# Performance work log

Hardware: AMD Instinct MI355X
Metric: run time of the kernel (lower is better)

The kernel has to match this reference:

```python
import jax, jax.numpy as jnp
import numpy as np
from math import sqrt

P = 1.0  # axis-aligned transform exponent (init arg p)
EPS = 1e-6


def setup_inputs() -> dict:
    key = jax.random.key(0)
    k1, k2, k3, k4 = jax.random.split(key, 4)
    B, L, S, H, E = 4, 2048, 2048, 8, 64
    return {
        "queries": jax.random.normal(k1, (B, L, H, E), dtype=jnp.float32),
        "keys": jax.random.normal(k2, (B, S, H, E), dtype=jnp.float32),
        "values": jax.random.normal(k3, (B, S, H, E), dtype=jnp.float32),
        "attn_mask": jnp.zeros((1, 1, 1, 1), dtype=bool),  # unused: mask_flag=False
        "directional_weights": jnp.ones((1, 1, 1, 1), dtype=jnp.float32),
        "dynamic_param": jax.random.normal(k4, (1,), dtype=jnp.float32),
    }


def _transform(x, directional_weights, dynamic_param):
    # axis_aligned_transformation: rescale by (1/std over seq dim)^p (unbiased std, like torch)
    std = jnp.std(x, axis=-2, keepdims=True, ddof=1)
    x = x * (1.0 / (std + EPS)) ** P
    # directional_reweighting then nonlinear_mapping
    x = x * directional_weights
    return jnp.tanh(x) * dynamic_param


def reference(queries, keys, values, attn_mask, directional_weights, dynamic_param):
    B, L, H, E = queries.shape
    scale = 1.0 / sqrt(E)
    qt = _transform(queries, directional_weights, dynamic_param)  # [B,L,H,E]
    kt = _transform(keys, directional_weights, dynamic_param)     # [B,S,H,E]
    scores = jnp.einsum('blhe,bshe->bhls', qt, kt)                # [B,H,L,S]
    # per-row tau = sqrt(var(scores) + eps), unbiased variance like torch.var
    tau = jnp.sqrt(jnp.var(scores, axis=-1, keepdims=True, ddof=1) + EPS)
    A = jax.nn.softmax(scale * scores / tau, axis=-1)             # [B,H,L,S]
    V = jnp.einsum('bhls,bshd->blhd', A, values)                  # [B,L,H,D]
    return V
```

## Files before the change

kernel.cpp:

```cpp
#include <hip/hip_runtime.h>
#include <math.h>

#define B_ 4
#define L_ 2048
#define S_ 2048
#define H_ 8
#define E_ 64
#define BH_ (B_*H_)
#define EPS 1e-6f
#define LOG2E 1.44269504088896340736f

typedef __attribute__((ext_vector_type(8))) short short8;
typedef __attribute__((ext_vector_type(4))) float f32x4;

__device__ __forceinline__ unsigned short f2bf(float f) {
    unsigned int u = __float_as_uint(f);
    u = (u + 0x7fffu + ((u >> 16) & 1u)) >> 16;
    return (unsigned short)u;
}

__device__ __forceinline__ float bf2f(unsigned short u) {
    return __uint_as_float(((unsigned int)u) << 16);
}

__device__ __forceinline__ float fast_tanh(float x) {
    float e = __expf(2.0f * x);
    return 1.0f - 2.0f / (e + 1.0f);
}

__device__ __forceinline__ unsigned int cvt_pk_bf16(float lo, float hi) {
    unsigned int r;
    asm("v_cvt_pk_bf16_f32 %0, %1, %2" : "=v"(r) : "v"(lo), "v"(hi));
    return r;
}
__device__ __forceinline__ float exp2_fast(float x) {
    float r;
    asm("v_exp_f32 %0, %1" : "=v"(r) : "v"(x));
    return r;
}
__device__ __forceinline__ void swap32(unsigned int &a, unsigned int &b) {
    asm("v_permlane32_swap_b32 %0, %1" : "+v"(a), "+v"(b));
}
__device__ __forceinline__ void swap16(unsigned int &a, unsigned int &b) {
    asm("v_permlane16_swap_b32 %0, %1" : "+v"(a), "+v"(b));
}

__device__ __forceinline__ int swb(int row, int byteoff) {
    return row * 128 + ((((byteoff >> 4) ^ (row & 7)) << 4) | (byteoff & 15));
}

__global__ __launch_bounds__(256) void pre_kernel(
    const float* __restrict__ xq, const float* __restrict__ xk,
    const float* __restrict__ xv,
    unsigned short* __restrict__ qt, unsigned short* __restrict__ kt,
    unsigned short* __restrict__ vt,
    const float* __restrict__ dwp, const float* __restrict__ dpp)
{
    __shared__ float ls[64][65];
    int bx = blockIdx.x;
    if (bx < 4096) {
        const float* x = (bx < 2048) ? xq : xk;
        unsigned short* xt = (bx < 2048) ? qt : kt;
        int g = (bx & 2047) * 256 + threadIdx.x;
        int e = g & 63;
        int bl = g >> 6;
        int b = bl >> 11;
        int l = bl & 2047;
        size_t base = (size_t)bl * (H_ * E_) + e;
        float v[8], s = 0.f, q = 0.f;
#pragma unroll
        for (int h = 0; h < 8; ++h) {
            float t = x[base + h * E_];
            v[h] = t; s += t; q += t * t;
        }
        float mean = s * 0.125f;
        float var = (q - s * mean) * (1.f / 7.f);
        var = fmaxf(var, 0.f);
        float inv = 1.f / (sqrtf(var) + EPS);
        float wsc = dwp[0] * inv;
        float d = dpp[0];
#pragma unroll
        for (int h = 0; h < 8; ++h) {
            float t = fast_tanh(v[h] * wsc) * d;
            xt[((size_t)(b * H_ + h) * L_ + l) * E_ + e] = f2bf(t);
        }
    } else {
        int t2 = bx - 4096;
        int s0 = (t2 & 31) * 64;
        int h = (t2 >> 5) & 7, b = t2 >> 8;
        int t = threadIdx.x;
#pragma unroll
        for (int i = 0; i < 4; ++i) {
            int idx = t + i * 256;
            int r = idx >> 4, c4 = (idx & 15) * 4;
            const float4 f = *(const float4*)&xv[((size_t)(b * S_ + s0 + r) * H_ + h) * E_ + c4];
            ls[r][c4] = f.x; ls[r][c4 + 1] = f.y; ls[r][c4 + 2] = f.z; ls[r][c4 + 3] = f.w;
        }
        __syncthreads();
        size_t ob = ((size_t)(b * H_ + h) * (S_ / 64) + (s0 >> 6)) * 4096;
#pragma unroll
        for (int i = 0; i < 2; ++i) {
            int ri = t + i * 256;
            int et = ri >> 7, c = (ri >> 6) & 1, quad = (ri >> 4) & 3, m = ri & 15;
            int e = et * 16 + m, sb = c * 32 + quad * 8;
            unsigned short tmp[8];
#pragma unroll
            for (int j = 0; j < 8; ++j) tmp[j] = f2bf(ls[sb + j][e]);
            *(uint4*)&vt[ob + (size_t)ri * 8] = *(uint4*)tmp;
        }
    }
}

__global__ __launch_bounds__(256) void gram_kernel(
    const unsigned short* __restrict__ kt, unsigned short* __restrict__ Gb,
    float* __restrict__ ksum)
{
    __shared__ unsigned short ks[128 * 72];
    __shared__ float gs[4096];
    __shared__ float kss[64];
    int bh = blockIdx.x;
    const unsigned short* base = kt + (size_t)bh * S_ * E_;
    int tid = threadIdx.x, lane = tid & 63, w = tid >> 6;
    int m = lane & 15, quad = lane >> 4;

    f32x4 acc[4][4];
#pragma unroll
    for (int i = 0; i < 4; ++i)
#pragma unroll
        for (int j = 0; j < 4; ++j) acc[i][j] = (f32x4){0.f, 0.f, 0.f, 0.f};
    float ksp[4] = {0.f, 0.f, 0.f, 0.f};

    short8 stg[4];
#pragma unroll
    for (int i = 0; i < 4; ++i)
        stg[i] = *(const short8*)(base + (size_t)(tid + i * 256) * 8);

    for (int ch = 0; ch < 16; ++ch) {
        __syncthreads();
#pragma unroll
        for (int i = 0; i < 4; ++i) {
            int u = tid + i * 256;
            *(short8*)&ks[(u >> 3) * 72 + (u & 7) * 8] = stg[i];
        }
        __syncthreads();
        if (ch < 15) {
#pragma unroll
            for (int i = 0; i < 4; ++i)
                stg[i] = *(const short8*)(base + (size_t)(ch + 1) * 8192 + (tid + i * 256) * 8);
        }
        int s0 = w * 32;
        short8 af[4];
#pragma unroll
        for (int i = 0; i < 4; ++i) {
            short8 a;
#pragma unroll
            for (int kk = 0; kk < 8; ++kk) {
                unsigned short uv = ks[(s0 + quad * 8 + kk) * 72 + i * 16 + m];
                a[kk] = (short)uv;
                ksp[i] += bf2f(uv);
            }
            af[i] = a;
        }
#pragma unroll
        for (int i = 0; i < 4; ++i)
#pragma unroll
            for (int j = 0; j < 4; ++j)
                acc[i][j] = __builtin_amdgcn_mfma_f32_16x16x32_bf16(af[i], af[j], acc[i][j], 0, 0, 0);
    }
#pragma unroll
    for (int i = 0; i < 4; ++i) {
        ksp[i] += __shfl_xor(ksp[i], 16);
        ksp[i] += __shfl_xor(ksp[i], 32);
    }
    for (int w2 = 0; w2 < 4; ++w2) {
        if (w == w2) {
#pragma unroll
            for (int i = 0; i < 4; ++i)
#pragma unroll
                for (int j = 0; j < 4; ++j)
#pragma unroll
                    for (int r = 0; r < 4; ++r) {
                        int idx = (i * 16 + quad * 4 + r) * 64 + j * 16 + m;
                        if (w2 == 0) gs[idx] = acc[i][j][r]; else gs[idx] += acc[i][j][r];
                    }
            if (lane < 16) {
#pragma unroll
                for (int i = 0; i < 4; ++i) {
                    int e = i * 16 + lane;
                    if (w2 == 0) kss[e] = ksp[i]; else kss[e] += ksp[i];
                }
            }
        }
        __syncthreads();
    }
#pragma unroll
    for (int ii = 0; ii < 16; ++ii) {
        int idx = tid + ii * 256;
        Gb[(size_t)bh * 4096 + idx] = f2bf(gs[idx]);
    }
    if (tid < 64) ksum[bh * 64 + tid] = kss[tid];
}

__global__ __launch_bounds__(512, 4) void attn_kernel(
    const unsigned short* __restrict__ qt,
    const unsigned short* __restrict__ kt,
    const unsigned short* __restrict__ vt,
    const unsigned short* __restrict__ Gb,
    const float* __restrict__ ksum,
    float* __restrict__ out)
{
    __shared__ __align__(16) char lds[17408];
    const int tid = threadIdx.x;
    const int lane = tid & 63;
    const int w = tid >> 6;
    const int m = lane & 15;
    const int quad = lane >> 4;
    float2* ascr = (float2*)(lds + 16384) + w * 16;

    int blk = blockIdx.x;
    int bh = (blk & 7) * 4 + ((blk >> 3) & 3);
    int l0 = (blk >> 5) * 128;
    int b = bh >> 3, h = bh & 7;

    const unsigned short* qtb = qt + (size_t)bh * L_ * E_;
    const unsigned short* ktb = kt + (size_t)bh * S_ * E_;
    const unsigned short* vtb = vt + (size_t)bh * (S_ / 64) * 4096;

    short8 qf[2];
#pragma unroll
    for (int c = 0; c < 2; ++c)
        qf[c] = *(const short8*)(qtb + (size_t)(l0 + w * 16 + m) * E_ + c * 32 + quad * 8);

    float al2, nalm2;
    {
        const unsigned short* gb = Gb + (size_t)bh * 4096;
        short8 gfr[4][2];
#pragma unroll
        for (int j = 0; j < 4; ++j)
#pragma unroll
            for (int c = 0; c < 2; ++c)
                gfr[j][c] = *(const short8*)(gb + (size_t)(j * 16 + m) * 64 + c * 32 + quad * 8);
        float ksl[4];
#pragma unroll
        for (int j = 0; j < 4; ++j) ksl[j] = ksum[bh * 64 + j * 16 + m];
        f32x4 accj[4];
#pragma unroll
        for (int j = 0; j < 4; ++j) {
            accj[j] = (f32x4){0.f, 0.f, 0.f, 0.f};
            accj[j] = __builtin_amdgcn_mfma_f32_16x16x32_bf16(qf[0], gfr[j][0], accj[j], 0, 0, 0);
            accj[j] = __builtin_amdgcn_mfma_f32_16x16x32_bf16(qf[1], gfr[j][1], accj[j], 0, 0, 0);
        }
        float ps[4] = {0, 0, 0, 0}, pr[4] = {0, 0, 0, 0};
#pragma unroll
        for (int r = 0; r < 4; ++r)
#pragma unroll
            for (int j = 0; j < 4; ++j) {
                float qv = bf2f(qtb[(size_t)(l0 + w * 16 + quad * 4 + r) * E_ + j * 16 + m]);
                ps[r] = fmaf(accj[j][r], qv, ps[r]);
                pr[r] = fmaf(qv, ksl[j], pr[r]);
            }
#pragma unroll
        for (int mask = 1; mask < 16; mask <<= 1)
#pragma unroll
            for (int r = 0; r < 4; ++r) {
                ps[r] += __shfl_xor(ps[r], mask);
                pr[r] += __shfl_xor(pr[r], mask);
            }
        if (m == 0) {
#pragma unroll
            for (int r = 0; r < 4; ++r) {
                float sum = pr[r];
                float mu = sum * (1.f / S_);
                float var = (ps[r] - sum * mu) * (1.f / (S_ - 1));
                var = fmaxf(var, 0.f);
                float tau = sqrtf(var + EPS);
                float a = 0.125f / tau;
                ascr[quad * 4 + r] = make_float2(a, a * mu);
            }
        }
        float2 a2 = ascr[m];
        al2 = a2.x * LOG2E; nalm2 = -a2.y * LOG2E;
    }

    f32x4 oacc[4];
#pragma unroll
    for (int et = 0; et < 4; ++et) oacc[et] = (f32x4){0.f, 0.f, 0.f, 0.f};
    f32x4 asum = (f32x4){0.f, 0.f, 0.f, 0.f};

    short8 ones;
#pragma unroll
    for (int j = 0; j < 8; ++j) ones[j] = (short)0x3F80;

    int ko[4];
#pragma unroll
    for (int nt = 0; nt < 4; ++nt)
        ko[nt] = swb(nt * 16 + m, quad * 16);
    const int stg = swb(tid >> 3, (tid & 7) * 16);

    uint4 kr = *(const uint4*)(ktb + (size_t)tid * 8);
    *(uint4*)(lds + stg) = kr;
    __syncthreads();

    auto step = [&](int st, char* kcur, char* knxt) {
        if (st < S_ / 64 - 1)
            kr = *(const uint4*)(ktb + (size_t)(st + 1) * 4096 + (size_t)tid * 8);
        const unsigned short* vstb = vtb + (size_t)st * 4096;
        short8 vf[2][4];
#pragma unroll
        for (int c = 0; c < 2; ++c)
#pragma unroll
            for (int et = 0; et < 4; ++et)
                vf[c][et] = *(const short8*)(vstb + et * 1024 + c * 512 + lane * 8);

        unsigned int W[4][2];
#pragma unroll
        for (int nt = 0; nt < 4; ++nt) {
            short8 kf0 = *(const short8*)(kcur + ko[nt]);
            short8 kf1 = *(const short8*)(kcur + (ko[nt] ^ 64));
            f32x4 acc = (f32x4){0.f, 0.f, 0.f, 0.f};
            acc = __builtin_amdgcn_mfma_f32_16x16x32_bf16(kf0, qf[0], acc, 0, 0, 0);
            acc = __builtin_amdgcn_mfma_f32_16x16x32_bf16(kf1, qf[1], acc, 0, 0, 0);
            float p0 = exp2_fast(fmaf(al2, acc[0], nalm2));
            float p1 = exp2_fast(fmaf(al2, acc[1], nalm2));
            float p2 = exp2_fast(fmaf(al2, acc[2], nalm2));
            float p3 = exp2_fast(fmaf(al2, acc[3], nalm2));
            W[nt][0] = cvt_pk_bf16(p0, p1);
            W[nt][1] = cvt_pk_bf16(p2, p3);
        }
        short8 pf[2];
#pragma unroll
        for (int c = 0; c < 2; ++c) {
            unsigned int a0 = W[2 * c][0], b0 = W[2 * c + 1][0];
            unsigned int a1 = W[2 * c][1], b1 = W[2 * c + 1][1];
            swap32(a0, b0); swap16(a0, b0);
            swap32(a1, b1); swap16(a1, b1);
            uint4 pk4;
            pk4.x = a0; pk4.y = a1; pk4.z = b0; pk4.w = b1;
            pf[c] = *(short8*)&pk4;
        }
#pragma unroll
        for (int et = 0; et < 4; ++et) {
            oacc[et] = __builtin_amdgcn_mfma_f32_16x16x32_bf16(pf[0], vf[0][et], oacc[et], 0, 0, 0);
            oacc[et] = __builtin_amdgcn_mfma_f32_16x16x32_bf16(pf[1], vf[1][et], oacc[et], 0, 0, 0);
        }
        asum = __builtin_amdgcn_mfma_f32_16x16x32_bf16(pf[0], ones, asum, 0, 0, 0);
        asum = __builtin_amdgcn_mfma_f32_16x16x32_bf16(pf[1], ones, asum, 0, 0, 0);
        if (st < S_ / 64 - 1)
            *(uint4*)(knxt + stg) = kr;
        __syncthreads();
    };
#pragma unroll 1
    for (int st2 = 0; st2 < S_ / 128; ++st2) {
        step(2 * st2,     lds,        lds + 8192);
        step(2 * st2 + 1, lds + 8192, lds);
    }

#pragma unroll
    for (int r = 0; r < 4; ++r) {
        float rd = 1.0f / asum[r];
        size_t row = (size_t)(b * L_ + l0 + w * 16 + quad * 4 + r);
#pragma unroll
        for (int et = 0; et < 4; ++et)
            out[(row * H_ + h) * E_ + et * 16 + m] = oacc[et][r] * rd;
    }
}

extern "C" void kernel_launch(void* const* d_in, const int* in_sizes, int n_in,
                              void* d_out, int out_size, void* d_ws, size_t ws_size,
                              hipStream_t stream)
{
    const float* q = (const float*)d_in[0];
    const float* k = (const float*)d_in[1];
    const float* v = (const float*)d_in[2];
    const float* dw = (const float*)d_in[4];
    const float* dp = (const float*)d_in[5];
    float* out = (float*)d_out;

    unsigned short* qt = (unsigned short*)d_ws;
    unsigned short* kt = qt + (size_t)BH_ * L_ * E_;
    unsigned short* vt = kt + (size_t)BH_ * S_ * E_;
    unsigned short* Gb = vt + (size_t)BH_ * E_ * S_;
    float* ksum = (float*)(Gb + (size_t)BH_ * 4096);

    pre_kernel<<<5120, 256, 0, stream>>>(q, k, v, qt, kt, vt, dw, dp);
    gram_kernel<<<BH_, 256, 0, stream>>>(kt, Gb, ksum);
    attn_kernel<<<512, 512, 0, stream>>>(qt, kt, vt, Gb, ksum, out);
}
```

Measured before the change: 168.8 us.

## Pre-swizzle K into MFMA fragment order and drop LDS staging in attention

The gram kernel now also writes K back in place in MFMA-fragment order. This lets the attention kernel load K fragments directly from global memory instead of staging them through double-buffered LDS with a barrier per step. Each wave now processes 32 query rows (two 16-row groups), so each K/V fragment load is reused twice, and blocks shrink to 256 threads. The pre kernel is also rewritten to use float4 loads and wave shuffles for the per-head std reduction, with packed bf16 stores. The risks are more redundant K traffic from L2 per wave, higher register pressure from the doubled accumulators, and an in-place layout rewrite that must stay ordered correctly within the gram kernel.

```diff
diff --git a/kernel.cpp b/kernel.cpp
--- a/kernel.cpp
+++ b/kernel.cpp
@@ -43,10 +43,6 @@
 }
 __device__ __forceinline__ void swap16(unsigned int &a, unsigned int &b) {
     asm("v_permlane16_swap_b32 %0, %1" : "+v"(a), "+v"(b));
-}
-
-__device__ __forceinline__ int swb(int row, int byteoff) {
-    return row * 128 + ((((byteoff >> 4) ^ (row & 7)) << 4) | (byteoff & 15));
 }
 
 __global__ __launch_bounds__(256) void pre_kernel(
@@ -58,37 +54,50 @@
 {
     __shared__ float ls[64][65];
     int bx = blockIdx.x;
+    int tid = threadIdx.x;
     if (bx < 4096) {
         const float* x = (bx < 2048) ? xq : xk;
         unsigned short* xt = (bx < 2048) ? qt : kt;
-        int g = (bx & 2047) * 256 + threadIdx.x;
-        int e = g & 63;
-        int bl = g >> 6;
-        int b = bl >> 11;
-        int l = bl & 2047;
-        size_t base = (size_t)bl * (H_ * E_) + e;
-        float v[8], s = 0.f, q = 0.f;
-#pragma unroll
-        for (int h = 0; h < 8; ++h) {
-            float t = x[base + h * E_];
-            v[h] = t; s += t; q += t * t;
-        }
-        float mean = s * 0.125f;
-        float var = (q - s * mean) * (1.f / 7.f);
-        var = fmaxf(var, 0.f);
-        float inv = 1.f / (sqrtf(var) + EPS);
-        float wsc = dwp[0] * inv;
-        float d = dpp[0];
-#pragma unroll
-        for (int h = 0; h < 8; ++h) {
-            float t = fast_tanh(v[h] * wsc) * d;
-            xt[((size_t)(b * H_ + h) * L_ + l) * E_ + e] = f2bf(t);
-        }
+        int wv = tid >> 6, ln = tid & 63;
+        int bl = (bx & 2047) * 4 + wv;
+        int b = bl >> 11, l = bl & 2047;
+        const float* xb = x + (size_t)bl * 512;
+        float4 fa = *(const float4*)(xb + ln * 4);
+        float4 fb = *(const float4*)(xb + 256 + ln * 4);
+        float s0 = fa.x + fb.x, s1 = fa.y + fb.y, s2 = fa.z + fb.z, s3 = fa.w + fb.w;
+        float q0 = fa.x * fa.x + fb.x * fb.x, q1 = fa.y * fa.y + fb.y * fb.y;
+        float q2 = fa.z * fa.z + fb.z * fb.z, q3 = fa.w * fa.w + fb.w * fb.w;
+        s0 += __shfl_xor(s0, 16); s1 += __shfl_xor(s1, 16);
+        s2 += __shfl_xor(s2, 16); s3 += __shfl_xor(s3, 16);
+        q0 += __shfl_xor(q0, 16); q1 += __shfl_xor(q1, 16);
+        q2 += __shfl_xor(q2, 16); q3 += __shfl_xor(q3, 16);
+        s0 += __shfl_xor(s0, 32); s1 += __shfl_xor(s1, 32);
+        s2 += __shfl_xor(s2, 32); s3 += __shfl_xor(s3, 32);
+        q0 += __shfl_xor(q0, 32); q1 += __shfl_xor(q1, 32);
+        q2 += __shfl_xor(q2, 32); q3 += __shfl_xor(q3, 32);
+        float dw = dwp[0], d = dpp[0];
+        auto mkw = [&](float s, float q) {
+            float mean = s * 0.125f;
+            float var = (q - s * mean) * (1.f / 7.f);
+            var = fmaxf(var, 0.f);
+            return dw / (sqrtf(var) + EPS);
+        };
+        float w0 = mkw(s0, q0), w1 = mkw(s1, q1), w2 = mkw(s2, q2), w3 = mkw(s3, q3);
+        float ta0 = fast_tanh(fa.x * w0) * d, ta1 = fast_tanh(fa.y * w1) * d;
+        float ta2 = fast_tanh(fa.z * w2) * d, ta3 = fast_tanh(fa.w * w3) * d;
+        float tb0 = fast_tanh(fb.x * w0) * d, tb1 = fast_tanh(fb.y * w1) * d;
+        float tb2 = fast_tanh(fb.z * w2) * d, tb3 = fast_tanh(fb.w * w3) * d;
+        uint2 pa, pb;
+        pa.x = cvt_pk_bf16(ta0, ta1); pa.y = cvt_pk_bf16(ta2, ta3);
+        pb.x = cvt_pk_bf16(tb0, tb1); pb.y = cvt_pk_bf16(tb2, tb3);
+        int hh = ln >> 4, e0 = (ln & 15) * 4;
+        *(uint2*)(xt + ((size_t)(b * 8 + hh) * 2048 + l) * 64 + e0) = pa;
+        *(uint2*)(xt + ((size_t)(b * 8 + hh + 4) * 2048 + l) * 64 + e0) = pb;
     } else {
         int t2 = bx - 4096;
         int s0 = (t2 & 31) * 64;
         int h = (t2 >> 5) & 7, b = t2 >> 8;
-        int t = threadIdx.x;
+        int t = tid;
 #pragma unroll
         for (int i = 0; i < 4; ++i) {
             int idx = t + i * 256;
@@ -112,14 +121,14 @@
 }
 
 __global__ __launch_bounds__(256) void gram_kernel(
-    const unsigned short* __restrict__ kt, unsigned short* __restrict__ Gb,
+    unsigned short* __restrict__ kt, unsigned short* __restrict__ Gb,
     float* __restrict__ ksum)
 {
     __shared__ unsigned short ks[128 * 72];
     __shared__ float gs[4096];
     __shared__ float kss[64];
     int bh = blockIdx.x;
-    const unsigned short* base = kt + (size_t)bh * S_ * E_;
+    unsigned short* base = kt + (size_t)bh * S_ * E_;
     int tid = threadIdx.x, lane = tid & 63, w = tid >> 6;
     int m = lane & 15, quad = lane >> 4;
 
@@ -148,6 +157,16 @@
             for (int i = 0; i < 4; ++i)
                 stg[i] = *(const short8*)(base + (size_t)(ch + 1) * 8192 + (tid + i * 256) * 8);
         }
+#pragma unroll
+        for (int tt = 0; tt < 2; ++tt)
+#pragma unroll
+            for (int i = 0; i < 2; ++i) {
+                int u = tid + i * 256;
+                int nt = u >> 7, cc = (u >> 6) & 1, ln2 = u & 63;
+                int mm = ln2 & 15, qq = ln2 >> 4;
+                short8 vv = *(const short8*)&ks[(tt * 64 + nt * 16 + mm) * 72 + cc * 32 + qq * 8];
+                *(uint4*)&base[(size_t)(ch * 2 + tt) * 4096 + (size_t)u * 8] = *(uint4*)&vv;
+            }
         int s0 = w * 32;
         short8 af[4];
 #pragma unroll
@@ -201,21 +220,21 @@
     if (tid < 64) ksum[bh * 64 + tid] = kss[tid];
 }
 
-__global__ __launch_bounds__(512, 4) void attn_kernel(
+__global__ __launch_bounds__(256, 2) void attn_kernel(
     const unsigned short* __restrict__ qt,
-    const unsigned short* __restrict__ kt,
+    const unsigned short* __restrict__ ktf,
     const unsigned short* __restrict__ vt,
     const unsigned short* __restrict__ Gb,
     const float* __restrict__ ksum,
     float* __restrict__ out)
 {
-    __shared__ __align__(16) char lds[17408];
+    __shared__ float2 ascr_s[4 * 32];
     const int tid = threadIdx.x;
     const int lane = tid & 63;
     const int w = tid >> 6;
     const int m = lane & 15;
     const int quad = lane >> 4;
-    float2* ascr = (float2*)(lds + 16384) + w * 16;
+    float2* ascr = ascr_s + w * 32;
 
     int blk = blockIdx.x;
     int bh = (blk & 7) * 4 + ((blk >> 3) & 3);
@@ -223,15 +242,17 @@
     int b = bh >> 3, h = bh & 7;
 
     const unsigned short* qtb = qt + (size_t)bh * L_ * E_;
-    const unsigned short* ktb = kt + (size_t)bh * S_ * E_;
+    const unsigned short* kb  = ktf + (size_t)bh * S_ * E_;
     const unsigned short* vtb = vt + (size_t)bh * (S_ / 64) * 4096;
 
-    short8 qf[2];
-#pragma unroll
-    for (int c = 0; c < 2; ++c)
-        qf[c] = *(const short8*)(qtb + (size_t)(l0 + w * 16 + m) * E_ + c * 32 + quad * 8);
-
-    float al2, nalm2;
+    short8 qf[2][2];
+#pragma unroll
+    for (int g = 0; g < 2; ++g)
+#pragma unroll
+        for (int c = 0; c < 2; ++c)
+            qf[g][c] = *(const short8*)(qtb + (size_t)(l0 + w * 32 + g * 16 + m) * E_ + c * 32 + quad * 8);
+
+    float al2[2], nalm2[2];
     {
         const unsigned short* gb = Gb + (size_t)bh * 4096;
         short8 gfr[4][2];
@@ -243,68 +264,74 @@
         float ksl[4];
 #pragma unroll
         for (int j = 0; j < 4; ++j) ksl[j] = ksum[bh * 64 + j * 16 + m];
-        f32x4 accj[4];
-#pragma unroll
-        for (int j = 0; j < 4; ++j) {
-            accj[j] = (f32x4){0.f, 0.f, 0.f, 0.f};
-            accj[j] = __builtin_amdgcn_mfma_f32_16x16x32_bf16(qf[0], gfr[j][0], accj[j], 0, 0, 0);
-            accj[j] = __builtin_amdgcn_mfma_f32_16x16x32_bf16(qf[1], gfr[j][1], accj[j], 0, 0, 0);
-        }
-        float ps[4] = {0, 0, 0, 0}, pr[4] = {0, 0, 0, 0};
-#pragma unroll
-        for (int r = 0; r < 4; ++r)
+#pragma unroll
+        for (int g = 0; g < 2; ++g) {
+            f32x4 accj[4];
 #pragma unroll
             for (int j = 0; j < 4; ++j) {
-                float qv = bf2f(qtb[(size_t)(l0 + w * 16 + quad * 4 + r) * E_ + j * 16 + m]);
-                ps[r] = fmaf(accj[j][r], qv, ps[r]);
-                pr[r] = fmaf(qv, ksl[j], pr[r]);
-            }
-#pragma unroll
-        for (int mask = 1; mask < 16; mask <<= 1)
-#pragma unroll
-            for (int r = 0; r < 4; ++r) {
-                ps[r] += __shfl_xor(ps[r], mask);
-                pr[r] += __shfl_xor(pr[r], mask);
-            }
-        if (m == 0) {
-#pragma unroll
-            for (int r = 0; r < 4; ++r) {
-                float sum = pr[r];
-                float mu = sum * (1.f / S_);
-                float var = (ps[r] - sum * mu) * (1.f / (S_ - 1));
-                var = fmaxf(var, 0.f);
-                float tau = sqrtf(var + EPS);
-                float a = 0.125f / tau;
-                ascr[quad * 4 + r] = make_float2(a, a * mu);
-            }
-        }
-        float2 a2 = ascr[m];
-        al2 = a2.x * LOG2E; nalm2 = -a2.y * LOG2E;
-    }
-
-    f32x4 oacc[4];
-#pragma unroll
-    for (int et = 0; et < 4; ++et) oacc[et] = (f32x4){0.f, 0.f, 0.f, 0.f};
-    f32x4 asum = (f32x4){0.f, 0.f, 0.f, 0.f};
+                accj[j] = (f32x4){0.f, 0.f, 0.f, 0.f};
+                accj[j] = __builtin_amdgcn_mfma_f32_16x16x32_bf16(qf[g][0], gfr[j][0], accj[j], 0, 0, 0);
+                accj[j] = __builtin_amdgcn_mfma_f32_16x16x32_bf16(qf[g][1], gfr[j][1], accj[j], 0, 0, 0);
+            }
+            float ps[4] = {0, 0, 0, 0}, pr[4] = {0, 0, 0, 0};
+#pragma unroll
+            for (int r = 0; r < 4; ++r)
+#pragma unroll
+                for (int j = 0; j < 4; ++j) {
+                    float qv = bf2f(qtb[(size_t)(l0 + w * 32 + g * 16 + quad * 4 + r) * E_ + j * 16 + m]);
+                    ps[r] = fmaf(accj[j][r], qv, ps[r]);
+                    pr[r] = fmaf(qv, ksl[j], pr[r]);
+                }
+#pragma unroll
+            for (int mask = 1; mask < 16; mask <<= 1)
+#pragma unroll
+                for (int r = 0; r < 4; ++r) {
+                    ps[r] += __shfl_xor(ps[r], mask);
+                    pr[r] += __shfl_xor(pr[r], mask);
+                }
+            if (m == 0) {
+#pragma unroll
+                for (int r = 0; r < 4; ++r) {
+                    float sum = pr[r];
+                    float mu = sum * (1.f / S_);
+                    float var = (ps[r] - sum * mu) * (1.f / (S_ - 1));
+                    var = fmaxf(var, 0.f);
+                    float tau = sqrtf(var + EPS);
+                    float a = 0.125f / tau;
+                    ascr[g * 16 + quad * 4 + r] = make_float2(a, a * mu);
+                }
+            }
+        }
+#pragma unroll
+        for (int g = 0; g < 2; ++g) {
+            float2 a2 = ascr[g * 16 + m];
+            al2[g] = a2.x * LOG2E; nalm2[g] = -a2.y * LOG2E;
+        }
+    }
+
+    f32x4 oacc[2][4];
+#pragma unroll
+    for (int g = 0; g < 2; ++g)
+#pragma unroll
+        for (int et = 0; et < 4; ++et) oacc[g][et] = (f32x4){0.f, 0.f, 0.f, 0.f};
+    f32x4 asum2[2];
+#pragma unroll
+    for (int g = 0; g < 2; ++g) asum2[g] = (f32x4){0.f, 0.f, 0.f, 0.f};
 
     short8 ones;
 #pragma unroll
     for (int j = 0; j < 8; ++j) ones[j] = (short)0x3F80;
 
-    int ko[4];
-#pragma unroll
-    for (int nt = 0; nt < 4; ++nt)
-        ko[nt] = swb(nt * 16 + m, quad * 16);
-    const int stg = swb(tid >> 3, (tid & 7) * 16);
-
-    uint4 kr = *(const uint4*)(ktb + (size_t)tid * 8);
-    *(uint4*)(lds + stg) = kr;
-    __syncthreads();
-
-    auto step = [&](int st, char* kcur, char* knxt) {
-        if (st < S_ / 64 - 1)
-            kr = *(const uint4*)(ktb + (size_t)(st + 1) * 4096 + (size_t)tid * 8);
+#pragma unroll 2
+    for (int st = 0; st < S_ / 64; ++st) {
+        const unsigned short* kstb = kb + (size_t)st * 4096;
         const unsigned short* vstb = vtb + (size_t)st * 4096;
+        short8 kf[4][2];
+#pragma unroll
+        for (int nt = 0; nt < 4; ++nt)
+#pragma unroll
+            for (int c = 0; c < 2; ++c)
+                kf[nt][c] = *(const short8*)(kstb + (nt * 2 + c) * 512 + lane * 8);
         short8 vf[2][4];
 #pragma unroll
         for (int c = 0; c < 2; ++c)
@@ -312,57 +339,54 @@
             for (int et = 0; et < 4; ++et)
                 vf[c][et] = *(const short8*)(vstb + et * 1024 + c * 512 + lane * 8);
 
-        unsigned int W[4][2];
-#pragma unroll
-        for (int nt = 0; nt < 4; ++nt) {
-            short8 kf0 = *(const short8*)(kcur + ko[nt]);
-            short8 kf1 = *(const short8*)(kcur + (ko[nt] ^ 64));
-            f32x4 acc = (f32x4){0.f, 0.f, 0.f, 0.f};
-            acc = __builtin_amdgcn_mfma_f32_16x16x32_bf16(kf0, qf[0], acc, 0, 0, 0);
-            acc = __builtin_amdgcn_mfma_f32_16x16x32_bf16(kf1, qf[1], acc, 0, 0, 0);
-            float p0 = exp2_fast(fmaf(al2, acc[0], nalm2));
-            float p1 = exp2_fast(fmaf(al2, acc[1], nalm2));
-            float p2 = exp2_fast(fmaf(al2, acc[2], nalm2));
-            float p3 = exp2_fast(fmaf(al2, acc[3], nalm2));
-            W[nt][0] = cvt_pk_bf16(p0, p1);
-            W[nt][1] = cvt_pk_bf16(p2, p3);
-        }
-        short8 pf[2];
-#pragma unroll
-        for (int c = 0; c < 2; ++c) {
-            unsigned int a0 = W[2 * c][0], b0 = W[2 * c + 1][0];
-            unsigned int a1 = W[2 * c][1], b1 = W[2 * c + 1][1];
-            swap32(a0, b0); swap16(a0, b0);
-            swap32(a1, b1); swap16(a1, b1);
-            uint4 pk4;
-            pk4.x = a0; pk4.y = a1; pk4.z = b0; pk4.w = b1;
-            pf[c] = *(short8*)&pk4;
-        }
-#pragma unroll
-        for (int et = 0; et < 4; ++et) {
-            oacc[et] = __builtin_amdgcn_mfma_f32_16x16x32_bf16(pf[0], vf[0][et], oacc[et], 0, 0, 0);
-            oacc[et] = __builtin_amdgcn_mfma_f32_16x16x32_bf16(pf[1], vf[1][et], oacc[et], 0, 0, 0);
-        }
-        asum = __builtin_amdgcn_mfma_f32_16x16x32_bf16(pf[0], ones, asum, 0, 0, 0);
-        asum = __builtin_amdgcn_mfma_f32_16x16x32_bf16(pf[1], ones, asum, 0, 0, 0);
-        if (st < S_ / 64 - 1)
-            *(uint4*)(knxt + stg) = kr;
-        __syncthreads();
-    };
-#pragma unroll 1
-    for (int st2 = 0; st2 < S_ / 128; ++st2) {
-        step(2 * st2,     lds,        lds + 8192);
-        step(2 * st2 + 1, lds + 8192, lds);
-    }
-
-#pragma unroll
-    for (int r = 0; r < 4; ++r) {
-        float rd = 1.0f / asum[r];
-        size_t row = (size_t)(b * L_ + l0 + w * 16 + quad * 4 + r);
-#pragma unroll
-        for (int et = 0; et < 4; ++et)
-            out[(row * H_ + h) * E_ + et * 16 + m] = oacc[et][r] * rd;
-    }
+        unsigned int W[2][4][2];
+#pragma unroll
+        for (int nt = 0; nt < 4; ++nt)
+#pragma unroll
+            for (int g = 0; g < 2; ++g) {
+                f32x4 acc = (f32x4){0.f, 0.f, 0.f, 0.f};
+                acc = __builtin_amdgcn_mfma_f32_16x16x32_bf16(kf[nt][0], qf[g][0], acc, 0, 0, 0);
+                acc = __builtin_amdgcn_mfma_f32_16x16x32_bf16(kf[nt][1], qf[g][1], acc, 0, 0, 0);
+                float p0 = exp2_fast(fmaf(al2[g], acc[0], nalm2[g]));
+                float p1 = exp2_fast(fmaf(al2[g], acc[1], nalm2[g]));
+                float p2 = exp2_fast(fmaf(al2[g], acc[2], nalm2[g]));
+                float p3 = exp2_fast(fmaf(al2[g], acc[3], nalm2[g]));
+                W[g][nt][0] = cvt_pk_bf16(p0, p1);
+                W[g][nt][1] = cvt_pk_bf16(p2, p3);
+            }
+#pragma unroll
+        for (int g = 0; g < 2; ++g) {
+            short8 pf[2];
+#pragma unroll
+            for (int c = 0; c < 2; ++c) {
+                unsigned int a0 = W[g][2 * c][0], b0 = W[g][2 * c + 1][0];
+                unsigned int a1 = W[g][2 * c][1], b1 = W[g][2 * c + 1][1];
+                swap32(a0, b0); swap16(a0, b0);
+                swap32(a1, b1); swap16(a1, b1);
+                uint4 pk4;
+                pk4.x = a0; pk4.y = a1; pk4.z = b0; pk4.w = b1;
+                pf[c] = *(short8*)&pk4;
+            }
+#pragma unroll
+            for (int et = 0; et < 4; ++et) {
+                oacc[g][et] = __builtin_amdgcn_mfma_f32_16x16x32_bf16(pf[0], vf[0][et], oacc[g][et], 0, 0, 0);
+                oacc[g][et] = __builtin_amdgcn_mfma_f32_16x16x32_bf16(pf[1], vf[1][et], oacc[g][et], 0, 0, 0);
+            }
+            asum2[g] = __builtin_amdgcn_mfma_f32_16x16x32_bf16(pf[0], ones, asum2[g], 0, 0, 0);
+            asum2[g] = __builtin_amdgcn_mfma_f32_16x16x32_bf16(pf[1], ones, asum2[g], 0, 0, 0);
+        }
+    }
+
+#pragma unroll
+    for (int g = 0; g < 2; ++g)
+#pragma unroll
+        for (int r = 0; r < 4; ++r) {
+            float rd = 1.0f / asum2[g][r];
+            size_t row = (size_t)(b * L_ + l0 + w * 32 + g * 16 + quad * 4 + r);
+#pragma unroll
+            for (int et = 0; et < 4; ++et)
+                out[(row * H_ + h) * E_ + et * 16 + m] = oacc[g][et][r] * rd;
+        }
 }
 
 extern "C" void kernel_launch(void* const* d_in, const int* in_sizes, int n_in,
@@ -384,5 +408,5 @@
 
     pre_kernel<<<5120, 256, 0, stream>>>(q, k, v, qt, kt, vt, dw, dp);
     gram_kernel<<<BH_, 256, 0, stream>>>(kt, Gb, ksum);
-    attn_kernel<<<512, 512, 0, stream>>>(qt, kt, vt, Gb, ksum, out);
-}
+    attn_kernel<<<512, 256, 0, stream>>>(qt, kt, vt, Gb, ksum, out);
+}
```

New measurement: 163.4 us. 1.03x faster.
